# Optimization experiments

Measured on AMD Instinct MI355X. Metric: run time of the kernel, lower is better.

Reference implementation:

```python
import math
import jax, jax.numpy as jnp
import numpy as np

TAU = 1.0
EPS = 1e-6


def _make_projection(m, d, seed=0):
    # FAVOR+ projection: stacked orthogonal d x d blocks (QR of gaussian),
    # rows rescaled by norms of gaussian rows (scaling=0 in the torch code).
    rng = np.random.default_rng(seed)
    blocks = []
    nb_full = m // d
    for _ in range(nb_full):
        q, _ = np.linalg.qr(rng.standard_normal((d, d)))
        blocks.append(q.T)
    rem = m - nb_full * d
    if rem > 0:
        q, _ = np.linalg.qr(rng.standard_normal((d, d)))
        blocks.append(q.T[:rem])
    mat = np.vstack(blocks)
    mult = np.linalg.norm(rng.standard_normal((m, d)), axis=1)
    return jnp.asarray((mult[:, None] * mat).astype(np.float32))


def setup_inputs() -> dict:
    B, N, H, D, d, m = 16, 4096, 8, 64, 64, 128
    key = jax.random.key(0)
    k1, k2, k3 = jax.random.split(key, 3)
    return {
        "x": jax.random.normal(k1, (B, N, H, D), jnp.float32),
        "node_vec1": jax.random.normal(k2, (B, N, H, d), jnp.float32),
        "node_vec2": jax.random.normal(k3, (B, N, H, d), jnp.float32),
        "proj": _make_projection(m, d),
    }


def _feature_map(data, proj, is_query):
    # data: [B,N,H,d], proj: [m,d]
    d = data.shape[-1]
    data = data * (1.0 / jnp.sqrt(jnp.sqrt(jnp.float32(d))))
    ratio = 1.0 / jnp.sqrt(jnp.float32(proj.shape[0]))
    data_dash = jnp.einsum('bnhd,md->bnhm', data, proj)
    diag = 0.5 * jnp.sum(data * data, axis=-1, keepdims=True)  # [B,N,H,1]
    if is_query:
        mx = jnp.max(data_dash, axis=-1, keepdims=True)
    else:
        # max over feature dim then over sequence/node dim (axis 1)
        mx = jnp.max(jnp.max(data_dash, axis=-1, keepdims=True), axis=1, keepdims=True)
    return ratio * (jnp.exp(data_dash - diag - mx) + EPS)


def reference(x, node_vec1, node_vec2, proj):
    inv_sqrt_tau = 1.0 / math.sqrt(TAU)
    v1p = _feature_map(node_vec1 * inv_sqrt_tau, proj, True)   # [B,N,H,m]
    v2p = _feature_map(node_vec2 * inv_sqrt_tau, proj, False)  # [B,N,H,m]
    # linear (kernelized) attention: O(N) in sequence length
    v2x = jnp.einsum('bnhm,bnhd->bhmd', v2p, x)                 # [B,H,m,D]
    out1 = jnp.einsum('bnhm,bhmd->bnhd', v1p, v2x)              # [B,N,H,D]
    v2_sum = jnp.sum(v2p, axis=1)                               # [B,H,m]
    out2 = jnp.einsum('bnhm,bhm->bnh', v1p, v2_sum)[..., None]  # [B,N,H,1]
    return (out1 / out2, v1p, v2p)
```

## Files before the change

### kernel.cpp

```cpp
#include <hip/hip_runtime.h>
#include <math.h>

constexpr int CN = 4096, CHH = 8, CD = 64, CM = 128;
constexpr int V1P_OFF = 16 * 4096 * 8 * 64;
constexpr int V2P_OFF = V1P_OFF + 16 * 4096 * 8 * 128;
constexpr float KSCALE = 0.35355339059327373f;
constexpr float KRATIO = 0.08838834764831843f;
constexpr float KEPS   = 1e-6f;

typedef __attribute__((ext_vector_type(8))) short bf16x8;
typedef __attribute__((ext_vector_type(4))) float f32x4;

__device__ __forceinline__ float dot4(float4 a, float4 b) {
  return fmaf(a.x, b.x, fmaf(a.y, b.y, fmaf(a.z, b.z, a.w * b.w)));
}
__device__ __forceinline__ float4 scl4(float4 a, float s) {
  return make_float4(a.x * s, a.y * s, a.z * s, a.w * s);
}
__device__ __forceinline__ short bhi(float f) {
  return (short)(__float_as_uint(f) >> 16);
}
__device__ __forceinline__ float bf2f(short s) {
  return __uint_as_float(((unsigned)(unsigned short)s) << 16);
}
__device__ __forceinline__ void split8(float4 u, float4 v, bf16x8& hi, bf16x8& lo) {
  float a[8] = {u.x, u.y, u.z, u.w, v.x, v.y, v.z, v.w};
#pragma unroll
  for (int e = 0; e < 8; e++) {
    short h = bhi(a[e]);
    hi[e] = h;
    lo[e] = bhi(a[e] - bf2f(h));
  }
}
__device__ __forceinline__ void split8a(const float* a, bf16x8& hi, bf16x8& lo) {
#pragma unroll
  for (int e = 0; e < 8; e++) {
    short h = bhi(a[e]);
    hi[e] = h;
    lo[e] = bhi(a[e] - bf2f(h));
  }
}

#define MFMA_B16(A, B, C) __builtin_amdgcn_mfma_f32_16x16x32_bf16(A, B, C, 0, 0, 0)

#define LOAD_BFRAGS(proj, lm, ko)                                   \
  bf16x8 Bh0[8], Bl0[8], Bh1[8], Bl1[8];                            \
  _Pragma("unroll")                                                 \
  for (int t = 0; t < 8; t++) {                                     \
    const float* pb = (proj) + (t * 16 + (lm)) * 64 + (ko);         \
    float4 p0 = *(const float4*)(pb);                               \
    float4 p1 = *(const float4*)(pb + 4);                           \
    float4 p2 = *(const float4*)(pb + 32);                          \
    float4 p3 = *(const float4*)(pb + 36);                          \
    split8(p0, p1, Bh0[t], Bl0[t]);                                 \
    split8(p2, p3, Bh1[t], Bl1[t]);                                 \
  }

template <int ROWMAX>
__global__ __launch_bounds__(256) void kp_stat(
    const float* __restrict__ inp, const float* __restrict__ proj,
    float* __restrict__ outmax) {
  const int l = threadIdx.x & 63, w = threadIdx.x >> 6;
  const int lm = l & 15, lk = l >> 4, ko = lk * 8;
  LOAD_BFRAGS(proj, lm, ko);
  const int bh = blockIdx.x >> 3, ch = blockIdx.x & 7;
  const int b = bh >> 3, h = bh & 7;
  float bmax = -1e30f;
  for (int s = 0; s < 8; s++) {
    const int nb = ch * 512 + w * 128 + s * 16;
    const size_t rA = (size_t)((b * CN + nb + lm) * CHH + h);
    const float* pa = inp + rA * 64 + ko;
    float4 a0 = scl4(*(const float4*)(pa), KSCALE);
    float4 a1 = scl4(*(const float4*)(pa + 4), KSCALE);
    float4 a2 = scl4(*(const float4*)(pa + 32), KSCALE);
    float4 a3 = scl4(*(const float4*)(pa + 36), KSCALE);
    bf16x8 Ah0, Al0, Ah1, Al1;
    split8(a0, a1, Ah0, Al0);
    split8(a2, a3, Ah1, Al1);
    float rm[4] = {-1e30f, -1e30f, -1e30f, -1e30f};
#pragma unroll
    for (int t = 0; t < 8; t++) {
      f32x4 acc = {0.f, 0.f, 0.f, 0.f};
      acc = MFMA_B16(Ah0, Bh0[t], acc);
      acc = MFMA_B16(Ah1, Bh1[t], acc);
      acc = MFMA_B16(Al0, Bh0[t], acc);
      acc = MFMA_B16(Al1, Bh1[t], acc);
      acc = MFMA_B16(Ah0, Bl0[t], acc);
      acc = MFMA_B16(Ah1, Bl1[t], acc);
#pragma unroll
      for (int r = 0; r < 4; r++) rm[r] = fmaxf(rm[r], acc[r]);
    }
    if (ROWMAX) {
#pragma unroll
      for (int r = 0; r < 4; r++) {
        float v = rm[r];
        v = fmaxf(v, __shfl_xor(v, 1));
        v = fmaxf(v, __shfl_xor(v, 2));
        v = fmaxf(v, __shfl_xor(v, 4));
        v = fmaxf(v, __shfl_xor(v, 8));
        rm[r] = v;
      }
      if (lm == 0) {
        const int nrow = nb + lk * 4;
#pragma unroll
        for (int r = 0; r < 4; r++)
          outmax[(size_t)((b * CN + nrow + r) * CHH + h)] = rm[r];
      }
    } else {
      bmax = fmaxf(fmaxf(bmax, fmaxf(rm[0], rm[1])), fmaxf(rm[2], rm[3]));
    }
  }
  if (!ROWMAX) {
    float v = bmax;
#pragma unroll
    for (int d = 1; d < 64; d <<= 1) v = fmaxf(v, __shfl_xor(v, d));
    __shared__ float wred[4];
    if (l == 0) wred[w] = v;
    __syncthreads();
    if (threadIdx.x == 0)
      outmax[blockIdx.x] = fmaxf(fmaxf(wred[0], wred[1]), fmaxf(wred[2], wred[3]));
  }
}

__global__ void k2b_max(const float* __restrict__ partmax, float* __restrict__ wmax) {
  const int bh = threadIdx.x;
  float m = -1e30f;
#pragma unroll
  for (int c = 0; c < 8; c++) m = fmaxf(m, partmax[bh * 8 + c]);
  wmax[bh] = m;
}

template <int V1P>
__global__ __launch_bounds__(256) void kp_emit(
    const float* __restrict__ inp, const float* __restrict__ proj,
    const float* __restrict__ mxin, float* __restrict__ outp) {
  const int l = threadIdx.x & 63, w = threadIdx.x >> 6;
  const int lm = l & 15, lk = l >> 4, ko = lk * 8;
  LOAD_BFRAGS(proj, lm, ko);
  const int bh = blockIdx.x >> 3, ch = blockIdx.x & 7;
  const int b = bh >> 3, h = bh & 7;
  const float whm = V1P ? 0.f : mxin[bh];
  for (int s = 0; s < 8; s++) {
    const int nb = ch * 512 + w * 128 + s * 16;
    const size_t rA = (size_t)((b * CN + nb + lm) * CHH + h);
    const float* pa = inp + rA * 64 + ko;
    float4 a0 = scl4(*(const float4*)(pa), KSCALE);
    float4 a1 = scl4(*(const float4*)(pa + 4), KSCALE);
    float4 a2 = scl4(*(const float4*)(pa + 32), KSCALE);
    float4 a3 = scl4(*(const float4*)(pa + 36), KSCALE);
    bf16x8 Ah0, Al0, Ah1, Al1;
    split8(a0, a1, Ah0, Al0);
    split8(a2, a3, Ah1, Al1);
    float dp = dot4(a0, a0) + dot4(a1, a1) + dot4(a2, a2) + dot4(a3, a3);
    dp += __shfl_xor(dp, 16);
    dp += __shfl_xor(dp, 32);
    float c[4];
    size_t obase[4];
#pragma unroll
    for (int r = 0; r < 4; r++) {
      const float dg = __shfl(dp, lk * 4 + r);
      const size_t rr = (size_t)((b * CN + nb + lk * 4 + r) * CHH + h);
      const float mxr = V1P ? mxin[rr] : whm;
      c[r] = -(0.5f * dg + mxr);
      obase[r] = rr * CM + lm;
    }
#pragma unroll
    for (int t = 0; t < 8; t++) {
      f32x4 acc = {0.f, 0.f, 0.f, 0.f};
      acc = MFMA_B16(Ah0, Bh0[t], acc);
      acc = MFMA_B16(Ah1, Bh1[t], acc);
      acc = MFMA_B16(Al0, Bh0[t], acc);
      acc = MFMA_B16(Al1, Bh1[t], acc);
      acc = MFMA_B16(Ah0, Bl0[t], acc);
      acc = MFMA_B16(Ah1, Bl1[t], acc);
#pragma unroll
      for (int r = 0; r < 4; r++)
        outp[obase[r] + t * 16] = KRATIO * (__expf(acc[r] + c[r]) + KEPS);
    }
  }
}

__global__ __launch_bounds__(256) void k3m(
    const float* __restrict__ v2p, const float* __restrict__ x,
    float* __restrict__ part, float* __restrict__ vsumpart) {
  const int l = threadIdx.x & 63, w = threadIdx.x >> 6;
  const int lm = l & 15, lk = l >> 4;
  const int bh = blockIdx.x >> 5, ch = blockIdx.x & 31;
  const int b = bh >> 3, h = bh & 7;
  const int jt0 = w * 2;
  f32x4 acc[2][4];
#pragma unroll
  for (int jj = 0; jj < 2; jj++)
#pragma unroll
    for (int dt = 0; dt < 4; dt++) acc[jj][dt] = (f32x4){0.f, 0.f, 0.f, 0.f};
  float vs0 = 0.f, vs1 = 0.f;
  for (int t = 0; t < 4; t++) {
    const int n0 = ch * 128 + t * 32 + lk * 8;
    bf16x8 Ah[2], Al[2];
#pragma unroll
    for (int jj = 0; jj < 2; jj++) {
      float af[8];
#pragma unroll
      for (int e = 0; e < 8; e++)
        af[e] = v2p[(size_t)((b * CN + n0 + e) * CHH + h) * CM + (jt0 + jj) * 16 + lm];
      split8a(af, Ah[jj], Al[jj]);
      float p = 0.f;
#pragma unroll
      for (int e = 0; e < 8; e++) p += af[e];
      if (jj == 0) vs0 += p; else vs1 += p;
    }
#pragma unroll
    for (int dt = 0; dt < 4; dt++) {
      float bfv[8];
#pragma unroll
      for (int e = 0; e < 8; e++)
        bfv[e] = x[(size_t)((b * CN + n0 + e) * CHH + h) * CD + dt * 16 + lm];
      bf16x8 Bh, Bl;
      split8a(bfv, Bh, Bl);
#pragma unroll
      for (int jj = 0; jj < 2; jj++) {
        acc[jj][dt] = MFMA_B16(Ah[jj], Bh, acc[jj][dt]);
        acc[jj][dt] = MFMA_B16(Al[jj], Bh, acc[jj][dt]);
        acc[jj][dt] = MFMA_B16(Ah[jj], Bl, acc[jj][dt]);
      }
    }
  }
  const size_t pbase = (size_t)blockIdx.x * 8192;
#pragma unroll
  for (int jj = 0; jj < 2; jj++)
#pragma unroll
    for (int dt = 0; dt < 4; dt++)
#pragma unroll
      for (int r = 0; r < 4; r++)
        part[pbase + ((size_t)(jt0 + jj) * 16 + lk * 4 + r) * 64 + dt * 16 + lm] = acc[jj][dt][r];
  float v0 = vs0, v1 = vs1;
  v0 += __shfl_xor(v0, 16); v0 += __shfl_xor(v0, 32);
  v1 += __shfl_xor(v1, 16); v1 += __shfl_xor(v1, 32);
  if (lk == 0) {
    vsumpart[(size_t)blockIdx.x * 128 + (jt0 + 0) * 16 + lm] = v0;
    vsumpart[(size_t)blockIdx.x * 128 + (jt0 + 1) * 16 + lm] = v1;
  }
}

__global__ void k3b_reduce(const float* __restrict__ part, const float* __restrict__ vsumpart,
                           float* __restrict__ v2x, float* __restrict__ vsum) {
  const int i = blockIdx.x * 256 + threadIdx.x;
  if (i < 1048576) {
    const int bh = i >> 13, r = i & 8191;
    float s = 0.f;
#pragma unroll
    for (int c = 0; c < 32; c++) s += part[(size_t)(bh * 32 + c) * 8192 + r];
    v2x[i] = s;
  } else if (i < 1048576 + 16384) {
    const int k = i - 1048576, bh = k >> 7, j = k & 127;
    float s = 0.f;
#pragma unroll
    for (int c = 0; c < 32; c++) s += vsumpart[(size_t)(bh * 32 + c) * 128 + j];
    vsum[k] = s;
  }
}

__global__ __launch_bounds__(256) void k4m(
    const float* __restrict__ v1p, const float* __restrict__ v2xg,
    const float* __restrict__ vsumg, float* __restrict__ out0) {
  const int l = threadIdx.x & 63, dt = threadIdx.x >> 6;
  const int lm = l & 15, lk = l >> 4;
  const int bh = blockIdx.x >> 4, ch = blockIdx.x & 15;
  const int b = bh >> 3, h = bh & 7;
  bf16x8 Bh[4], Bl[4];
#pragma unroll
  for (int kc = 0; kc < 4; kc++) {
    float bfv[8];
#pragma unroll
    for (int e = 0; e < 8; e++)
      bfv[e] = v2xg[(size_t)bh * 8192 + (size_t)(kc * 32 + lk * 8 + e) * 64 + dt * 16 + lm];
    split8a(bfv, Bh[kc], Bl[kc]);
  }
  float vsr[4][8];
#pragma unroll
  for (int kc = 0; kc < 4; kc++)
#pragma unroll
    for (int e = 0; e < 8; e++)
      vsr[kc][e] = vsumg[bh * 128 + kc * 32 + lk * 8 + e];
  for (int s = 0; s < 16; s++) {
    const int nb = ch * 256 + s * 16;
    const float* pa = v1p + (size_t)((b * CN + nb + lm) * CHH + h) * CM;
    bf16x8 Ah[4], Al[4];
    float o2p = 0.f;
#pragma unroll
    for (int kc = 0; kc < 4; kc++) {
      float4 u = *(const float4*)(pa + kc * 32 + lk * 8);
      float4 v = *(const float4*)(pa + kc * 32 + lk * 8 + 4);
      split8(u, v, Ah[kc], Al[kc]);
      o2p += u.x * vsr[kc][0] + u.y * vsr[kc][1] + u.z * vsr[kc][2] + u.w * vsr[kc][3]
           + v.x * vsr[kc][4] + v.y * vsr[kc][5] + v.z * vsr[kc][6] + v.w * vsr[kc][7];
    }
    o2p += __shfl_xor(o2p, 16);
    o2p += __shfl_xor(o2p, 32);
    f32x4 acc = {0.f, 0.f, 0.f, 0.f};
#pragma unroll
    for (int kc = 0; kc < 4; kc++) {
      acc = MFMA_B16(Ah[kc], Bh[kc], acc);
      acc = MFMA_B16(Al[kc], Bh[kc], acc);
      acc = MFMA_B16(Ah[kc], Bl[kc], acc);
    }
#pragma unroll
    for (int r = 0; r < 4; r++) {
      const float inv = 1.0f / __shfl(o2p, lk * 4 + r);
      out0[(size_t)((b * CN + nb + lk * 4 + r) * CHH + h) * CD + dt * 16 + lm] = acc[r] * inv;
    }
  }
}

extern "C" void kernel_launch(void* const* d_in, const int* in_sizes, int n_in,
                              void* d_out, int out_size, void* d_ws, size_t ws_size,
                              hipStream_t stream) {
  (void)in_sizes; (void)n_in; (void)out_size; (void)ws_size;
  const float* x    = (const float*)d_in[0];
  const float* nv1  = (const float*)d_in[1];
  const float* nv2  = (const float*)d_in[2];
  const float* proj = (const float*)d_in[3];
  float* out  = (float*)d_out;
  float* out0 = out;
  float* v1p  = out + V1P_OFF;
  float* v2p  = out + V2P_OFF;

  float* part     = v1p;
  float* vsumpart = v1p + 33554432;
  float* rowmax   = out0;
  float* ws      = (float*)d_ws;
  float* wmax    = ws;
  float* vsum    = ws + 128;
  float* v2x     = ws + 16512;
  float* partmax = ws + 16512 + 1048576;

  kp_stat<0><<<dim3(1024), dim3(256), 0, stream>>>(nv2, proj, partmax);
  k2b_max   <<<dim3(1),    dim3(128), 0, stream>>>(partmax, wmax);
  kp_emit<0><<<dim3(1024), dim3(256), 0, stream>>>(nv2, proj, wmax, v2p);
  k3m       <<<dim3(4096), dim3(256), 0, stream>>>(v2p, x, part, vsumpart);
  k3b_reduce<<<dim3(4160), dim3(256), 0, stream>>>(part, vsumpart, v2x, vsum);
  kp_stat<1><<<dim3(1024), dim3(256), 0, stream>>>(nv1, proj, rowmax);
  kp_emit<1><<<dim3(1024), dim3(256), 0, stream>>>(nv1, proj, rowmax, v1p);
  k4m       <<<dim3(2048), dim3(256), 0, stream>>>(v1p, v2x, vsum, out0);
}
```

Baseline: 607.1 us.

## Fuse v1p row-max and emit into one kernel; shrink k3m split-N partials

For the query feature map, the separate row-max pass and emit pass become one kernel. It keeps all eight MFMA accumulator tiles in registers, reduces the row max with lane shuffles, then applies the exp. This removes a full re-read of node_vec1, a second projection matmul and the rowmax round trip. The v2p·x kernel now gives each block 512 rows instead of 128, so it writes 4x fewer partials and the reduce kernel sums 8 chunks instead of 32. The cost is more registers for the held accumulators and less parallelism in k3m.

```diff
diff --git a/kernel.cpp b/kernel.cpp
--- a/kernel.cpp
+++ b/kernel.cpp
@@ -56,7 +56,16 @@
     split8(p2, p3, Bh1[t], Bl1[t]);                                 \
   }
 
-template <int ROWMAX>
+#define PROJ_MFMA(acc, t)                                           \
+  do {                                                              \
+    acc = MFMA_B16(Ah0, Bh0[t], acc);                               \
+    acc = MFMA_B16(Ah1, Bh1[t], acc);                               \
+    acc = MFMA_B16(Al0, Bh0[t], acc);                               \
+    acc = MFMA_B16(Al1, Bh1[t], acc);                               \
+    acc = MFMA_B16(Ah0, Bl0[t], acc);                               \
+    acc = MFMA_B16(Ah1, Bl1[t], acc);                               \
+  } while (0)
+
 __global__ __launch_bounds__(256) void kp_stat(
     const float* __restrict__ inp, const float* __restrict__ proj,
     float* __restrict__ outmax) {
@@ -81,45 +90,20 @@
 #pragma unroll
     for (int t = 0; t < 8; t++) {
       f32x4 acc = {0.f, 0.f, 0.f, 0.f};
-      acc = MFMA_B16(Ah0, Bh0[t], acc);
-      acc = MFMA_B16(Ah1, Bh1[t], acc);
-      acc = MFMA_B16(Al0, Bh0[t], acc);
-      acc = MFMA_B16(Al1, Bh1[t], acc);
-      acc = MFMA_B16(Ah0, Bl0[t], acc);
-      acc = MFMA_B16(Ah1, Bl1[t], acc);
+      PROJ_MFMA(acc, t);
 #pragma unroll
       for (int r = 0; r < 4; r++) rm[r] = fmaxf(rm[r], acc[r]);
     }
-    if (ROWMAX) {
-#pragma unroll
-      for (int r = 0; r < 4; r++) {
-        float v = rm[r];
-        v = fmaxf(v, __shfl_xor(v, 1));
-        v = fmaxf(v, __shfl_xor(v, 2));
-        v = fmaxf(v, __shfl_xor(v, 4));
-        v = fmaxf(v, __shfl_xor(v, 8));
-        rm[r] = v;
-      }
-      if (lm == 0) {
-        const int nrow = nb + lk * 4;
-#pragma unroll
-        for (int r = 0; r < 4; r++)
-          outmax[(size_t)((b * CN + nrow + r) * CHH + h)] = rm[r];
-      }
-    } else {
-      bmax = fmaxf(fmaxf(bmax, fmaxf(rm[0], rm[1])), fmaxf(rm[2], rm[3]));
-    }
-  }
-  if (!ROWMAX) {
-    float v = bmax;
-#pragma unroll
-    for (int d = 1; d < 64; d <<= 1) v = fmaxf(v, __shfl_xor(v, d));
-    __shared__ float wred[4];
-    if (l == 0) wred[w] = v;
-    __syncthreads();
-    if (threadIdx.x == 0)
-      outmax[blockIdx.x] = fmaxf(fmaxf(wred[0], wred[1]), fmaxf(wred[2], wred[3]));
-  }
+    bmax = fmaxf(fmaxf(bmax, fmaxf(rm[0], rm[1])), fmaxf(rm[2], rm[3]));
+  }
+  float v = bmax;
+#pragma unroll
+  for (int d = 1; d < 64; d <<= 1) v = fmaxf(v, __shfl_xor(v, d));
+  __shared__ float wred[4];
+  if (l == 0) wred[w] = v;
+  __syncthreads();
+  if (threadIdx.x == 0)
+    outmax[blockIdx.x] = fmaxf(fmaxf(wred[0], wred[1]), fmaxf(wred[2], wred[3]));
 }
 
 __global__ void k2b_max(const float* __restrict__ partmax, float* __restrict__ wmax) {
@@ -130,7 +114,6 @@
   wmax[bh] = m;
 }
 
-template <int V1P>
 __global__ __launch_bounds__(256) void kp_emit(
     const float* __restrict__ inp, const float* __restrict__ proj,
     const float* __restrict__ mxin, float* __restrict__ outp) {
@@ -139,7 +122,7 @@
   LOAD_BFRAGS(proj, lm, ko);
   const int bh = blockIdx.x >> 3, ch = blockIdx.x & 7;
   const int b = bh >> 3, h = bh & 7;
-  const float whm = V1P ? 0.f : mxin[bh];
+  const float whm = mxin[bh];
   for (int s = 0; s < 8; s++) {
     const int nb = ch * 512 + w * 128 + s * 16;
     const size_t rA = (size_t)((b * CN + nb + lm) * CHH + h);
@@ -160,22 +143,75 @@
     for (int r = 0; r < 4; r++) {
       const float dg = __shfl(dp, lk * 4 + r);
       const size_t rr = (size_t)((b * CN + nb + lk * 4 + r) * CHH + h);
-      const float mxr = V1P ? mxin[rr] : whm;
-      c[r] = -(0.5f * dg + mxr);
+      c[r] = -(0.5f * dg + whm);
       obase[r] = rr * CM + lm;
     }
 #pragma unroll
     for (int t = 0; t < 8; t++) {
       f32x4 acc = {0.f, 0.f, 0.f, 0.f};
-      acc = MFMA_B16(Ah0, Bh0[t], acc);
-      acc = MFMA_B16(Ah1, Bh1[t], acc);
-      acc = MFMA_B16(Al0, Bh0[t], acc);
-      acc = MFMA_B16(Al1, Bh1[t], acc);
-      acc = MFMA_B16(Ah0, Bl0[t], acc);
-      acc = MFMA_B16(Ah1, Bl1[t], acc);
+      PROJ_MFMA(acc, t);
 #pragma unroll
       for (int r = 0; r < 4; r++)
         outp[obase[r] + t * 16] = KRATIO * (__expf(acc[r] + c[r]) + KEPS);
+    }
+  }
+}
+
+__global__ __launch_bounds__(256) void kv1e(
+    const float* __restrict__ inp, const float* __restrict__ proj,
+    float* __restrict__ outp) {
+  const int l = threadIdx.x & 63, w = threadIdx.x >> 6;
+  const int lm = l & 15, lk = l >> 4, ko = lk * 8;
+  LOAD_BFRAGS(proj, lm, ko);
+  const int bh = blockIdx.x >> 3, ch = blockIdx.x & 7;
+  const int b = bh >> 3, h = bh & 7;
+  for (int s = 0; s < 8; s++) {
+    const int nb = ch * 512 + w * 128 + s * 16;
+    const size_t rA = (size_t)((b * CN + nb + lm) * CHH + h);
+    const float* pa = inp + rA * 64 + ko;
+    float4 a0 = scl4(*(const float4*)(pa), KSCALE);
+    float4 a1 = scl4(*(const float4*)(pa + 4), KSCALE);
+    float4 a2 = scl4(*(const float4*)(pa + 32), KSCALE);
+    float4 a3 = scl4(*(const float4*)(pa + 36), KSCALE);
+    bf16x8 Ah0, Al0, Ah1, Al1;
+    split8(a0, a1, Ah0, Al0);
+    split8(a2, a3, Ah1, Al1);
+    float dp = dot4(a0, a0) + dot4(a1, a1) + dot4(a2, a2) + dot4(a3, a3);
+    dp += __shfl_xor(dp, 16);
+    dp += __shfl_xor(dp, 32);
+    f32x4 acc8[8];
+#pragma unroll
+    for (int t = 0; t < 8; t++) {
+      f32x4 acc = {0.f, 0.f, 0.f, 0.f};
+      PROJ_MFMA(acc, t);
+      acc8[t] = acc;
+    }
+    float rm[4];
+#pragma unroll
+    for (int r = 0; r < 4; r++) {
+      float m = acc8[0][r];
+#pragma unroll
+      for (int t = 1; t < 8; t++) m = fmaxf(m, acc8[t][r]);
+      m = fmaxf(m, __shfl_xor(m, 1));
+      m = fmaxf(m, __shfl_xor(m, 2));
+      m = fmaxf(m, __shfl_xor(m, 4));
+      m = fmaxf(m, __shfl_xor(m, 8));
+      rm[r] = m;
+    }
+    float c[4];
+    size_t obase[4];
+#pragma unroll
+    for (int r = 0; r < 4; r++) {
+      const float dg = __shfl(dp, lk * 4 + r);
+      const size_t rr = (size_t)((b * CN + nb + lk * 4 + r) * CHH + h);
+      c[r] = -(0.5f * dg + rm[r]);
+      obase[r] = rr * CM + lm;
+    }
+#pragma unroll
+    for (int t = 0; t < 8; t++) {
+#pragma unroll
+      for (int r = 0; r < 4; r++)
+        outp[obase[r] + t * 16] = KRATIO * (__expf(acc8[t][r] + c[r]) + KEPS);
     }
   }
 }
@@ -185,7 +221,7 @@
     float* __restrict__ part, float* __restrict__ vsumpart) {
   const int l = threadIdx.x & 63, w = threadIdx.x >> 6;
   const int lm = l & 15, lk = l >> 4;
-  const int bh = blockIdx.x >> 5, ch = blockIdx.x & 31;
+  const int bh = blockIdx.x >> 3, ch = blockIdx.x & 7;
   const int b = bh >> 3, h = bh & 7;
   const int jt0 = w * 2;
   f32x4 acc[2][4];
@@ -194,8 +230,8 @@
 #pragma unroll
     for (int dt = 0; dt < 4; dt++) acc[jj][dt] = (f32x4){0.f, 0.f, 0.f, 0.f};
   float vs0 = 0.f, vs1 = 0.f;
-  for (int t = 0; t < 4; t++) {
-    const int n0 = ch * 128 + t * 32 + lk * 8;
+  for (int t = 0; t < 16; t++) {
+    const int n0 = ch * 512 + t * 32 + lk * 8;
     bf16x8 Ah[2], Al[2];
 #pragma unroll
     for (int jj = 0; jj < 2; jj++) {
@@ -249,13 +285,13 @@
     const int bh = i >> 13, r = i & 8191;
     float s = 0.f;
 #pragma unroll
-    for (int c = 0; c < 32; c++) s += part[(size_t)(bh * 32 + c) * 8192 + r];
+    for (int c = 0; c < 8; c++) s += part[(size_t)(bh * 8 + c) * 8192 + r];
     v2x[i] = s;
   } else if (i < 1048576 + 16384) {
     const int k = i - 1048576, bh = k >> 7, j = k & 127;
     float s = 0.f;
 #pragma unroll
-    for (int c = 0; c < 32; c++) s += vsumpart[(size_t)(bh * 32 + c) * 128 + j];
+    for (int c = 0; c < 8; c++) s += vsumpart[(size_t)(bh * 8 + c) * 128 + j];
     vsum[k] = s;
   }
 }
@@ -326,20 +362,18 @@
   float* v2p  = out + V2P_OFF;
 
   float* part     = v1p;
-  float* vsumpart = v1p + 33554432;
-  float* rowmax   = out0;
+  float* vsumpart = v1p + 8388608;
   float* ws      = (float*)d_ws;
   float* wmax    = ws;
   float* vsum    = ws + 128;
   float* v2x     = ws + 16512;
   float* partmax = ws + 16512 + 1048576;
 
-  kp_stat<0><<<dim3(1024), dim3(256), 0, stream>>>(nv2, proj, partmax);
+  kp_stat   <<<dim3(1024), dim3(256), 0, stream>>>(nv2, proj, partmax);
   k2b_max   <<<dim3(1),    dim3(128), 0, stream>>>(partmax, wmax);
-  kp_emit<0><<<dim3(1024), dim3(256), 0, stream>>>(nv2, proj, wmax, v2p);
-  k3m       <<<dim3(4096), dim3(256), 0, stream>>>(v2p, x, part, vsumpart);
+  kp_emit   <<<dim3(1024), dim3(256), 0, stream>>>(nv2, proj, wmax, v2p);
+  k3m       <<<dim3(1024), dim3(256), 0, stream>>>(v2p, x, part, vsumpart);
   k3b_reduce<<<dim3(4160), dim3(256), 0, stream>>>(part, vsumpart, v2x, vsum);
-  kp_stat<1><<<dim3(1024), dim3(256), 0, stream>>>(nv1, proj, rowmax);
-  kp_emit<1><<<dim3(1024), dim3(256), 0, stream>>>(nv1, proj, rowmax, v1p);
+  kv1e      <<<dim3(1024), dim3(256), 0, stream>>>(nv1, proj, v1p);
   k4m       <<<dim3(2048), dim3(256), 0, stream>>>(v1p, v2x, vsum, out0);
 }
```

Result: faster. 507.9 us (-16.3%).
